# Kernel tuning notes

Measured on AMD Instinct MI355X. Metric: run time of the kernel, lower is better.

The kernel has to match this reference:

```python
import jax, jax.numpy as jnp
import numpy as np

N_HEADS = 8
EPS = 1e-5

def _mha(q_in, kv_in, wq, bq, wk, bk, wv, bv, wo, bo, causal):
    B, N, D = q_in.shape
    Dh = D // N_HEADS
    # projections (weights stored [in, out])
    Q = (q_in @ wq + bq).reshape(B, N, N_HEADS, Dh).swapaxes(1, 2)  # [B,H,N,Dh]
    K = (kv_in @ wk + bk).reshape(B, N, N_HEADS, Dh).swapaxes(1, 2)
    V = (kv_in @ wv + bv).reshape(B, N, N_HEADS, Dh).swapaxes(1, 2)
    scores = jnp.einsum('bhqd,bhkd->bhqk', Q, K) / jnp.sqrt(jnp.asarray(Dh, q_in.dtype))
    if causal:
        m = jnp.triu(jnp.ones((N, N), dtype=bool), k=1)
        scores = jnp.where(m, jnp.asarray(-jnp.inf, scores.dtype), scores)
    w = jax.nn.softmax(scores, axis=-1)
    attn = jnp.einsum('bhqk,bhkd->bhqd', w, V).swapaxes(1, 2).reshape(B, N, D)
    return attn @ wo + bo

def _ln(x, g, b):
    mu = jnp.mean(x, axis=-1, keepdims=True)
    var = jnp.var(x, axis=-1, keepdims=True)
    return (x - mu) / jnp.sqrt(var + EPS) * g + b

def setup_inputs() -> dict:
    key = jax.random.key(0)
    D, H, S = 512, 8, 4
    ks = jax.random.split(key, 32)
    def w(k, shape):
        return jax.random.normal(k, shape, dtype=jnp.float32) * 0.02
    inp = {
        'x': jax.random.normal(ks[0], (2, 2048, D), dtype=jnp.float32),
        'encoder_output': jax.random.normal(ks[1], (2, 2048, D), dtype=jnp.float32),
        # masked self-attention params
        'm_wq': w(ks[2], (D, D)), 'm_bq': jnp.zeros((D,), jnp.float32),
        'm_wk': w(ks[3], (D, D)), 'm_bk': jnp.zeros((D,), jnp.float32),
        'm_wv': w(ks[4], (D, D)), 'm_bv': jnp.zeros((D,), jnp.float32),
        'm_wo': w(ks[5], (D, D)), 'm_bo': jnp.zeros((D,), jnp.float32),
        # cross-attention params
        'c_wq': w(ks[6], (D, D)), 'c_bq': jnp.zeros((D,), jnp.float32),
        'c_wk': w(ks[7], (D, D)), 'c_bk': jnp.zeros((D,), jnp.float32),
        'c_wv': w(ks[8], (D, D)), 'c_bv': jnp.zeros((D,), jnp.float32),
        'c_wo': w(ks[9], (D, D)), 'c_bo': jnp.zeros((D,), jnp.float32),
        # layer norms
        'ln1_g': jnp.ones((D,), jnp.float32), 'ln1_b': jnp.zeros((D,), jnp.float32),
        'ln2_g': jnp.ones((D,), jnp.float32), 'ln2_b': jnp.zeros((D,), jnp.float32),
        'ln3_g': jnp.ones((D,), jnp.float32), 'ln3_b': jnp.zeros((D,), jnp.float32),
        # feed-forward (scale=4)
        'ff_w1': w(ks[10], (D, S * D)), 'ff_b1': jnp.zeros((S * D,), jnp.float32),
        'ff_w2': w(ks[11], (S * D, D)), 'ff_b2': jnp.zeros((D,), jnp.float32),
    }
    return inp

def reference(x, encoder_output,
              m_wq, m_bq, m_wk, m_bk, m_wv, m_bv, m_wo, m_bo,
              c_wq, c_bq, c_wk, c_bk, c_wv, c_bv, c_wo, c_bo,
              ln1_g, ln1_b, ln2_g, ln2_b, ln3_g, ln3_b,
              ff_w1, ff_b1, ff_w2, ff_b2):
    x = _mha(x, x, m_wq, m_bq, m_wk, m_bk, m_wv, m_bv, m_wo, m_bo, causal=True) + x
    x = _ln(x, ln1_g, ln1_b)
    x = _mha(x, encoder_output, c_wq, c_bq, c_wk, c_bk, c_wv, c_bv, c_wo, c_bo, causal=False) + x
    x = _ln(x, ln2_g, ln2_b)
    h = jax.nn.gelu(x @ ff_w1 + ff_b1, approximate=False)  # torch nn.GELU default = exact erf
    x = h @ ff_w2 + ff_b2 + x
    x = _ln(x, ln3_g, ln3_b)
    return x
```

## Files before the change

kernel.cpp:

```cpp
#include <hip/hip_runtime.h>
#include <hip/hip_bf16.h>

typedef __attribute__((ext_vector_type(8))) short short8;
typedef __attribute__((ext_vector_type(4))) float floatx4;
typedef unsigned short u16;
typedef unsigned int u32;

#define QSCALE 0.1803368801111244f

__device__ __forceinline__ u16 f2b(float f) {
    union { float f; u32 u; } v; v.f = f;
    u32 r = v.u + 0x7fffu + ((v.u >> 16) & 1u);
    return (u16)(r >> 16);
}

__device__ __forceinline__ float b2f(u16 b) {
    u32 u = ((u32)b) << 16;
    union { u32 u; float f; } v; v.u = u;
    return v.f;
}

__device__ __forceinline__ u32 pk2(float a, float b) {
    __hip_bfloat162 w = __float22bfloat162_rn(make_float2(a, b));
    return *(u32*)&w;
}

__device__ __forceinline__ void gload(const u16* g, u16* l) {
    __builtin_amdgcn_global_load_lds((const __attribute__((address_space(1))) void*)g,
                                     (__attribute__((address_space(3))) void*)l, 16, 0, 0);
}

struct TPent { const float* s; u16* d; int O; int dI; };
struct TP16 { TPent e[16]; };
__global__ __launch_bounds__(256) void transpose_convert16(TP16 p) {
    __shared__ float t[32][33];
    TPent e = p.e[blockIdx.z];
    int o0 = blockIdx.x * 32, i0 = blockIdx.y * 32;
    int tx = threadIdx.x, ty = threadIdx.y;
#pragma unroll
    for (int k = 0; k < 32; k += 8) t[ty + k][tx] = e.s[(size_t)(i0 + ty + k) * e.O + o0 + tx];
    __syncthreads();
#pragma unroll
    for (int k = 0; k < 32; k += 8) e.d[(size_t)(o0 + ty + k) * e.dI + i0 + tx] = f2b(t[tx][ty + k]);
}

__global__ __launch_bounds__(256) void gather_bias(const float* b0, const float* b1, const float* b2,
                                                   const float* b3, const float* b4,
                                                   float* dqkv, float* dkv) {
    int i = blockIdx.x * 256 + threadIdx.x;
    if      (i < 512)  dqkv[i] = b0[i];
    else if (i < 1024) dqkv[i] = b1[i - 512];
    else if (i < 1536) dqkv[i] = b2[i - 1024];
    else if (i < 2048) dkv[i - 1536] = b3[i - 1536];
    else               dkv[i - 1536] = b4[i - 2048];
}

__global__ __launch_bounds__(256) void cvt_bf16_2(const float4* __restrict__ s0, ushort4* __restrict__ d0,
                                                  const float4* __restrict__ s1, ushort4* __restrict__ d1) {
    int i = blockIdx.x * 256 + threadIdx.x;
    float4 v = s0[i];
    ushort4 o; o.x = f2b(v.x); o.y = f2b(v.y); o.z = f2b(v.z); o.w = f2b(v.w);
    d0[i] = o;
    v = s1[i];
    o.x = f2b(v.x); o.y = f2b(v.y); o.z = f2b(v.z); o.w = f2b(v.w);
    d1[i] = o;
}

__global__ __launch_bounds__(256) void gemm64x128(
    const u16* __restrict__ A, int lda,
    const u16* __restrict__ B, int ldb,
    int K,
    const float* __restrict__ bias,
    const float* __restrict__ residual,
    float* __restrict__ out_f, u16* __restrict__ out_b,
    int out_stride, int scale_ncols, int gelu_flag)
{
    __shared__ u16 lA[64 * 64];
    __shared__ u16 lB[128 * 64];
    int tid = threadIdx.x, wave = tid >> 6, lane = tid & 63;
    int g4 = lane >> 4, c16 = lane & 15;
    int swz = (c16 & 7) << 3;
    int bm = blockIdx.x * 64, bn = blockIdx.y * 128;
    int wm = (wave >> 1) * 32, wn = (wave & 1) * 64;
    int srow = tid >> 3, skseg = ((tid & 7) * 8) ^ ((srow & 7) << 3);
    const u16* Ar = A + (size_t)(bm + srow) * lda + skseg;
    const u16* Br = B + (size_t)(bn + srow) * ldb + skseg;
    size_t a32 = (size_t)32 * lda, b32 = (size_t)32 * ldb;

    floatx4 acc[2][4];
#pragma unroll
    for (int i = 0; i < 2; i++)
#pragma unroll
        for (int j = 0; j < 4; j++) acc[i][j] = (floatx4){0.f, 0.f, 0.f, 0.f};

    for (int kt = 0; kt < K; kt += 64) {
        __syncthreads();
        gload(Ar + kt,           lA + wave * 512);
        gload(Ar + kt + a32,     lA + 2048 + wave * 512);
        gload(Br + kt,           lB + wave * 512);
        gload(Br + kt + b32,     lB + 2048 + wave * 512);
        gload(Br + kt + 2 * b32, lB + 4096 + wave * 512);
        gload(Br + kt + 3 * b32, lB + 6144 + wave * 512);
        __syncthreads();
        short8 aF[2][2], bF[2][4];
#pragma unroll
        for (int kk = 0; kk < 2; kk++) {
            int ko = (g4 * 8 + kk * 32) ^ swz;
#pragma unroll
            for (int i = 0; i < 2; i++) aF[kk][i] = *(const short8*)&lA[(wm + i * 16 + c16) * 64 + ko];
#pragma unroll
            for (int j = 0; j < 4; j++) bF[kk][j] = *(const short8*)&lB[(wn + j * 16 + c16) * 64 + ko];
        }
#pragma unroll
        for (int kk = 0; kk < 2; kk++)
#pragma unroll
            for (int i = 0; i < 2; i++)
#pragma unroll
                for (int j = 0; j < 4; j++)
                    acc[i][j] = __builtin_amdgcn_mfma_f32_16x16x32_bf16(aF[kk][i], bF[kk][j], acc[i][j], 0, 0, 0);
    }

#pragma unroll
    for (int i = 0; i < 2; i++) {
        int row0 = bm + wm + i * 16 + g4 * 4;
#pragma unroll
        for (int j = 0; j < 4; j++) {
            int col = bn + wn + j * 16 + c16;
            float bv = bias[col];
#pragma unroll
            for (int r = 0; r < 4; r++) {
                int row = row0 + r;
                float v = acc[i][j][r] + bv;
                if (col < scale_ncols) v *= QSCALE;
                if (gelu_flag) v = 0.5f * v * (1.f + erff(v * 0.70710678118654752f));
                if (residual) v += residual[(size_t)row * out_stride + col];
                if (out_f) out_f[(size_t)row * out_stride + col] = v;
                else       out_b[(size_t)row * out_stride + col] = f2b(v);
            }
        }
    }
}

__global__ __launch_bounds__(256) void gemm64x128_dual(
    const u16* __restrict__ A0, const u16* __restrict__ B0, const float* __restrict__ bias0,
    u16* __restrict__ out0, int ostride0, int scale0,
    const u16* __restrict__ A1, const u16* __restrict__ B1, const float* __restrict__ bias1,
    u16* __restrict__ out1, int ostride1,
    int ys, int K, int lda, int ldb)
{
    __shared__ u16 lA[64 * 64];
    __shared__ u16 lB[128 * 64];
    int tid = threadIdx.x, wave = tid >> 6, lane = tid & 63;
    int g4 = lane >> 4, c16 = lane & 15;
    int swz = (c16 & 7) << 3;
    int by = blockIdx.y;
    const u16* A; const u16* B; const float* bias; u16* out; int ostride, scaleN, bn;
    if (by < ys) { A = A0; B = B0; bias = bias0; out = out0; ostride = ostride0; scaleN = scale0; bn = by * 128; }
    else         { A = A1; B = B1; bias = bias1; out = out1; ostride = ostride1; scaleN = 0;      bn = (by - ys) * 128; }
    int bm = blockIdx.x * 64;
    int wm = (wave >> 1) * 32, wn = (wave & 1) * 64;
    int srow = tid >> 3, skseg = ((tid & 7) * 8) ^ ((srow & 7) << 3);
    const u16* Ar = A + (size_t)(bm + srow) * lda + skseg;
    const u16* Br = B + (size_t)(bn + srow) * ldb + skseg;
    size_t a32 = (size_t)32 * lda, b32 = (size_t)32 * ldb;

    floatx4 acc[2][4];
#pragma unroll
    for (int i = 0; i < 2; i++)
#pragma unroll
        for (int j = 0; j < 4; j++) acc[i][j] = (floatx4){0.f, 0.f, 0.f, 0.f};

    for (int kt = 0; kt < K; kt += 64) {
        __syncthreads();
        gload(Ar + kt,           lA + wave * 512);
        gload(Ar + kt + a32,     lA + 2048 + wave * 512);
        gload(Br + kt,           lB + wave * 512);
        gload(Br + kt + b32,     lB + 2048 + wave * 512);
        gload(Br + kt + 2 * b32, lB + 4096 + wave * 512);
        gload(Br + kt + 3 * b32, lB + 6144 + wave * 512);
        __syncthreads();
        short8 aF[2][2], bF[2][4];
#pragma unroll
        for (int kk = 0; kk < 2; kk++) {
            int ko = (g4 * 8 + kk * 32) ^ swz;
#pragma unroll
            for (int i = 0; i < 2; i++) aF[kk][i] = *(const short8*)&lA[(wm + i * 16 + c16) * 64 + ko];
#pragma unroll
            for (int j = 0; j < 4; j++) bF[kk][j] = *(const short8*)&lB[(wn + j * 16 + c16) * 64 + ko];
        }
#pragma unroll
        for (int kk = 0; kk < 2; kk++)
#pragma unroll
            for (int i = 0; i < 2; i++)
#pragma unroll
                for (int j = 0; j < 4; j++)
                    acc[i][j] = __builtin_amdgcn_mfma_f32_16x16x32_bf16(aF[kk][i], bF[kk][j], acc[i][j], 0, 0, 0);
    }

#pragma unroll
    for (int i = 0; i < 2; i++) {
        int row0 = bm + wm + i * 16 + g4 * 4;
#pragma unroll
        for (int j = 0; j < 4; j++) {
            int col = bn + wn + j * 16 + c16;
            float bv = bias[col];
#pragma unroll
            for (int r = 0; r < 4; r++) {
                float v = acc[i][j][r] + bv;
                if (col < scaleN) v *= QSCALE;
                out[(size_t)(row0 + r) * ostride + col] = f2b(v);
            }
        }
    }
}

__global__ __launch_bounds__(256) void gemm64x64(
    const u16* __restrict__ A, int lda,
    const u16* __restrict__ B, int ldb,
    int K,
    const float* __restrict__ bias,
    u16* __restrict__ out_b,
    int out_stride, int scale_ncols)
{
    __shared__ u16 lA[64 * 64];
    __shared__ u16 lB[64 * 64];
    int tid = threadIdx.x, wave = tid >> 6, lane = tid & 63;
    int g4 = lane >> 4, c16 = lane & 15;
    int swz = (c16 & 7) << 3;
    int bm = blockIdx.x * 64, bn = blockIdx.y * 64;
    int wm = wave * 16;
    int srow = tid >> 3, skseg = ((tid & 7) * 8) ^ ((srow & 7) << 3);
    const u16* Ar = A + (size_t)(bm + srow) * lda + skseg;
    const u16* Br = B + (size_t)(bn + srow) * ldb + skseg;
    size_t a32 = (size_t)32 * lda, b32 = (size_t)32 * ldb;

    floatx4 acc[4];
#pragma unroll
    for (int j = 0; j < 4; j++) acc[j] = (floatx4){0.f, 0.f, 0.f, 0.f};

    for (int kt = 0; kt < K; kt += 64) {
        __syncthreads();
        gload(Ar + kt,       lA + wave * 512);
        gload(Ar + kt + a32, lA + 2048 + wave * 512);
        gload(Br + kt,       lB + wave * 512);
        gload(Br + kt + b32, lB + 2048 + wave * 512);
        __syncthreads();
        short8 aF[2], bF[2][4];
#pragma unroll
        for (int kk = 0; kk < 2; kk++) {
            int ko = (g4 * 8 + kk * 32) ^ swz;
            aF[kk] = *(const short8*)&lA[(wm + c16) * 64 + ko];
#pragma unroll
            for (int j = 0; j < 4; j++) bF[kk][j] = *(const short8*)&lB[(j * 16 + c16) * 64 + ko];
        }
#pragma unroll
        for (int kk = 0; kk < 2; kk++)
#pragma unroll
            for (int j = 0; j < 4; j++)
                acc[j] = __builtin_amdgcn_mfma_f32_16x16x32_bf16(aF[kk], bF[kk][j], acc[j], 0, 0, 0);
    }

    int row0 = bm + wm + g4 * 4;
#pragma unroll
    for (int j = 0; j < 4; j++) {
        int col = bn + j * 16 + c16;
        float bv = bias[col];
#pragma unroll
        for (int r = 0; r < 4; r++) {
            int row = row0 + r;
            float v = acc[j][r] + bv;
            if (col < scale_ncols) v *= QSCALE;
            out_b[(size_t)row * out_stride + col] = f2b(v);
        }
    }
}

__global__ __launch_bounds__(256) void gemm64x64s(
    const u16* __restrict__ A, int lda,
    const u16* __restrict__ B, int ldb,
    int Ksub,
    const float* __restrict__ bias,
    const float* __restrict__ res_f,
    const u16* __restrict__ res_b,
    u16* __restrict__ out0, int out_stride)
{
    __shared__ u16 lA[64 * 64];
    __shared__ u16 lB[64 * 64];
    int tid = threadIdx.x, wave = tid >> 6, lane = tid & 63;
    int g4 = lane >> 4, c16 = lane & 15;
    int swz = (c16 & 7) << 3;
    int bm = blockIdx.x * 64, bn = blockIdx.y * 64, sp = blockIdx.z;
    int wm = wave * 16;
    int srow = tid >> 3;
    int skseg = (((tid & 7) * 8) ^ ((srow & 7) << 3)) + sp * Ksub;
    const u16* Ar = A + (size_t)(bm + srow) * lda + skseg;
    const u16* Br = B + (size_t)(bn + srow) * ldb + skseg;
    size_t a32 = (size_t)32 * lda, b32 = (size_t)32 * ldb;

    floatx4 acc[4];
#pragma unroll
    for (int j = 0; j < 4; j++) acc[j] = (floatx4){0.f, 0.f, 0.f, 0.f};

    for (int kt = 0; kt < Ksub; kt += 64) {
        __syncthreads();
        gload(Ar + kt,       lA + wave * 512);
        gload(Ar + kt + a32, lA + 2048 + wave * 512);
        gload(Br + kt,       lB + wave * 512);
        gload(Br + kt + b32, lB + 2048 + wave * 512);
        __syncthreads();
        short8 aF[2], bF[2][4];
#pragma unroll
        for (int kk = 0; kk < 2; kk++) {
            int ko = (g4 * 8 + kk * 32) ^ swz;
            aF[kk] = *(const short8*)&lA[(wm + c16) * 64 + ko];
#pragma unroll
            for (int j = 0; j < 4; j++) bF[kk][j] = *(const short8*)&lB[(j * 16 + c16) * 64 + ko];
        }
#pragma unroll
        for (int kk = 0; kk < 2; kk++)
#pragma unroll
            for (int j = 0; j < 4; j++)
                acc[j] = __builtin_amdgcn_mfma_f32_16x16x32_bf16(aF[kk], bF[kk][j], acc[j], 0, 0, 0);
    }

    u16* out = out0 + (size_t)sp * 4096 * 512;
    int row0 = bm + wm + g4 * 4;
#pragma unroll
    for (int j = 0; j < 4; j++) {
        int col = bn + j * 16 + c16;
        float bv = (sp == 0) ? bias[col] : 0.f;
#pragma unroll
        for (int r = 0; r < 4; r++) {
            int row = row0 + r;
            float v = acc[j][r] + bv;
            if (sp == 0) {
                if (res_f)      v += res_f[(size_t)row * out_stride + col];
                else if (res_b) v += b2f(res_b[(size_t)row * out_stride + col]);
            }
            out[(size_t)row * out_stride + col] = f2b(v);
        }
    }
}

__global__ __launch_bounds__(256) void attn_fused(
    const u16* __restrict__ Qp, int q_stride,
    const u16* __restrict__ Kp, int kv_stride,
    const u16* __restrict__ Vp,
    u16* __restrict__ Opart,
    float* __restrict__ Lpart,
    int causal)
{
    __shared__ u16 lK[64 * 72];
    __shared__ u16 lVT[64 * 72];
    int tid = threadIdx.x, wave = tid >> 6, lane = tid & 63;
    int g4 = lane >> 4, c16 = lane & 15;
    int id = blockIdx.x;
    int bh = (id & 7) | ((id >> 3 & 1) << 3);
    int rest = id >> 4;
    int qt = rest & 31;
    int sp = rest >> 5;
    if (causal) qt = 31 - qt;
    size_t rowbase = (size_t)(bh >> 3) * 2048;
    int hoff = (bh & 7) * 64;
    const u16* Q = Qp + rowbase * q_stride + hoff;
    const u16* K = Kp + rowbase * kv_stride + hoff;
    const u16* V = Vp + rowbase * kv_stride + hoff;

    int qrow0 = qt * 64 + wave * 16;
    short8 qf0 = *(const short8*)&Q[(size_t)(qrow0 + c16) * q_stride + g4 * 8];
    short8 qf1 = *(const short8*)&Q[(size_t)(qrow0 + c16) * q_stride + g4 * 8 + 32];

    int kr = tid >> 2, ks = (tid & 3) * 16;
    int krow = 16 * (2 * (kr >> 5) + ((kr >> 2) & 1)) + 4 * ((kr >> 3) & 3) + (kr & 3);
    const u16* Kbase = K + (size_t)kr * kv_stride + ks;
    int vk0 = (tid >> 3) * 2, vs = (tid & 7) * 8;
    const u16* Vbase = V + (size_t)vk0 * kv_stride + vs;

    int4 kv0, kv1, vv0, vv1;
    auto load_tile = [&](int kt) {
        const u16* kp = Kbase + (size_t)kt * 64 * kv_stride;
        kv0 = *(const int4*)(kp);
        kv1 = *(const int4*)(kp + 8);
        const u16* vp = Vbase + (size_t)kt * 64 * kv_stride;
        vv0 = *(const int4*)(vp);
        vv1 = *(const int4*)(vp + kv_stride);
    };
    auto store_tile = [&]() {
        *(int4*)&lK[krow * 72 + ks] = kv0;
        *(int4*)&lK[krow * 72 + ks + 8] = kv1;
        const u16* pa = (const u16*)&vv0;
        const u16* pb = (const u16*)&vv1;
#pragma unroll
        for (int j = 0; j < 8; j++) {
            int dh = vs + j;
            int keyS = vk0 ^ (((dh >> 3) & 3) << 4);
            u32 w = (u32)pa[j] | ((u32)pb[j] << 16);
            *(u32*)&lVT[dh * 72 + keyS] = w;
        }
    };

    floatx4 o_acc[4];
#pragma unroll
    for (int d = 0; d < 4; d++) o_acc[d] = (floatx4){0.f, 0.f, 0.f, 0.f};
    float lsum = 0.f;

    int ktend = causal ? (qt + 1) : 32;
    int kt = sp;
    if (kt < ktend) load_tile(kt);

    for (; kt < ktend; kt += 2) {
        __syncthreads();
        store_tile();
        __syncthreads();
        if (kt + 2 < ktend) load_tile(kt + 2);

        floatx4 sc[4];
#pragma unroll
        for (int nt = 0; nt < 4; nt++) {
            short8 b0 = *(const short8*)&lK[(nt * 16 + c16) * 72 + g4 * 8];
            short8 b1 = *(const short8*)&lK[(nt * 16 + c16) * 72 + g4 * 8 + 32];
            floatx4 z = (floatx4){0.f, 0.f, 0.f, 0.f};
            z = __builtin_amdgcn_mfma_f32_16x16x32_bf16(b0, qf0, z, 0, 0, 0);
            z = __builtin_amdgcn_mfma_f32_16x16x32_bf16(b1, qf1, z, 0, 0, 0);
            sc[nt] = z;
        }
        if (causal && kt == qt) {
            int qr = qt * 64 + wave * 16 + c16;
#pragma unroll
            for (int nt = 0; nt < 4; nt++) {
                int key0 = kt * 64 + 8 * g4 + 4 * (nt & 1) + 32 * (nt >> 1);
#pragma unroll
                for (int r = 0; r < 4; r++)
                    if (key0 + r > qr) sc[nt][r] = -1e30f;
            }
        }
        float e[4][4];
#pragma unroll
        for (int nt = 0; nt < 4; nt++) {
#pragma unroll
            for (int r = 0; r < 4; r++) {
                e[nt][r] = exp2f(sc[nt][r]);
                lsum += e[nt][r];
            }
        }
        short8 pa0, pa1;
        {
            u32 w[8];
            w[0] = pk2(e[0][0], e[0][1]); w[1] = pk2(e[0][2], e[0][3]);
            w[2] = pk2(e[1][0], e[1][1]); w[3] = pk2(e[1][2], e[1][3]);
            w[4] = pk2(e[2][0], e[2][1]); w[5] = pk2(e[2][2], e[2][3]);
            w[6] = pk2(e[3][0], e[3][1]); w[7] = pk2(e[3][2], e[3][3]);
            pa0 = *(short8*)&w[0];
            pa1 = *(short8*)&w[4];
        }
#pragma unroll
        for (int d = 0; d < 4; d++) {
            int swz = ((2 * d + (c16 >> 3)) & 3) << 4;
            short8 vb0 = *(const short8*)&lVT[(d * 16 + c16) * 72 + ((g4 * 8) ^ swz)];
            short8 vb1 = *(const short8*)&lVT[(d * 16 + c16) * 72 + ((32 + g4 * 8) ^ swz)];
            o_acc[d] = __builtin_amdgcn_mfma_f32_16x16x32_bf16(pa0, vb0, o_acc[d], 0, 0, 0);
            o_acc[d] = __builtin_amdgcn_mfma_f32_16x16x32_bf16(pa1, vb1, o_acc[d], 0, 0, 0);
        }
    }

    lsum += __shfl_xor(lsum, 16);
    lsum += __shfl_xor(lsum, 32);
    size_t slab = (size_t)(sp * 16 + bh) * 2048;
    if (g4 == 0) Lpart[slab + qrow0 + c16] = lsum;
    u16* Ob = Opart + (slab + qrow0) * 64;
#pragma unroll
    for (int d = 0; d < 4; d++)
#pragma unroll
        for (int r = 0; r < 4; r++)
            Ob[(size_t)(4 * g4 + r) * 64 + d * 16 + c16] = f2b(o_acc[d][r]);
}

__global__ __launch_bounds__(256) void attn_combine(
    const ushort4* __restrict__ Op,
    const float* __restrict__ Lp,
    ushort4* __restrict__ out)
{
    int e = blockIdx.x * 256 + threadIdx.x;
    int dh4 = e & 15;
    int qrow = (e >> 4) & 2047;
    int bh = e >> 15;
    int li = bh * 2048 + qrow;
    float l = Lp[li] + Lp[32768 + li];
    float inv = 1.f / l;
    ushort4 a = Op[e];
    ushort4 b = Op[524288 + e];
    ushort4 o;
    o.x = f2b((b2f(a.x) + b2f(b.x)) * inv);
    o.y = f2b((b2f(a.y) + b2f(b.y)) * inv);
    o.z = f2b((b2f(a.z) + b2f(b.z)) * inv);
    o.w = f2b((b2f(a.w) + b2f(b.w)) * inv);
    int row = (bh >> 3) * 2048 + qrow;
    out[(size_t)row * 128 + (bh & 7) * 16 + dh4] = o;
}

__global__ __launch_bounds__(256) void ln_kernel(const u16* __restrict__ in0,
                                                 const u16* __restrict__ in1,
                                                 const float* __restrict__ g,
                                                 const float* __restrict__ b,
                                                 float* __restrict__ out_f,
                                                 u16* __restrict__ out_b)
{
    const int D = 512;
    int row = blockIdx.x, tid = threadIdx.x;
    size_t base = (size_t)row * D;
    float v0 = b2f(in0[base + tid]) + b2f(in1[base + tid]);
    float v1 = b2f(in0[base + tid + 256]) + b2f(in1[base + tid + 256]);
    float s = v0 + v1, ss = v0 * v0 + v1 * v1;
#pragma unroll
    for (int off = 1; off < 64; off <<= 1) { s += __shfl_xor(s, off); ss += __shfl_xor(ss, off); }
    __shared__ float red[8];
    int wave = tid >> 6, lane = tid & 63;
    if (lane == 0) { red[wave] = s; red[4 + wave] = ss; }
    __syncthreads();
    float st = red[0] + red[1] + red[2] + red[3];
    float sst = red[4] + red[5] + red[6] + red[7];
    float mu = st * (1.f / 512.f);
    float var = sst * (1.f / 512.f) - mu * mu;
    float rs = rsqrtf(var + 1e-5f);
    float y0 = (v0 - mu) * rs * g[tid] + b[tid];
    float y1 = (v1 - mu) * rs * g[tid + 256] + b[tid + 256];
    if (out_f) { out_f[base + tid] = y0; out_f[base + tid + 256] = y1; }
    if (out_b) { out_b[base + tid] = f2b(y0); out_b[base + tid + 256] = f2b(y1); }
}

extern "C" void kernel_launch(void* const* d_in, const int* in_sizes, int n_in,
                              void* d_out, int out_size, void* d_ws, size_t ws_size,
                              hipStream_t stream)
{
    (void)in_sizes; (void)n_in; (void)out_size; (void)ws_size;
    const float* x     = (const float*)d_in[0];
    const float* enc   = (const float*)d_in[1];
    const float* m_wq  = (const float*)d_in[2];  const float* m_bq = (const float*)d_in[3];
    const float* m_wk  = (const float*)d_in[4];  const float* m_bk = (const float*)d_in[5];
    const float* m_wv  = (const float*)d_in[6];  const float* m_bv = (const float*)d_in[7];
    const float* m_wo  = (const float*)d_in[8];  const float* m_bo = (const float*)d_in[9];
    const float* c_wq  = (const float*)d_in[10]; const float* c_bq = (const float*)d_in[11];
    const float* c_wk  = (const float*)d_in[12]; const float* c_bk = (const float*)d_in[13];
    const float* c_wv  = (const float*)d_in[14]; const float* c_bv = (const float*)d_in[15];
    const float* c_wo  = (const float*)d_in[16]; const float* c_bo = (const float*)d_in[17];
    const float* ln1_g = (const float*)d_in[18]; const float* ln1_b = (const float*)d_in[19];
    const float* ln2_g = (const float*)d_in[20]; const float* ln2_b = (const float*)d_in[21];
    const float* ln3_g = (const float*)d_in[22]; const float* ln3_b = (const float*)d_in[23];
    const float* ff_w1 = (const float*)d_in[24]; const float* ff_b1 = (const float*)d_in[25];
    const float* ff_w2 = (const float*)d_in[26]; const float* ff_b2 = (const float*)d_in[27];

    char* base = (char*)d_ws; size_t off = 0;
    auto alloc = [&](size_t bytes) -> void* {
        void* p = base + off; off = (off + bytes + 255) & ~(size_t)255; return p;
    };
    u16*   Wqkv_m = (u16*)alloc(1536 * 512 * 2);
    u16*   Wo_m   = (u16*)alloc(512 * 512 * 2);
    u16*   Wq_c   = (u16*)alloc(512 * 512 * 2);
    u16*   Wkv_c  = (u16*)alloc(1024 * 512 * 2);
    u16*   Wo_c   = (u16*)alloc(512 * 512 * 2);
    u16*   W1t    = (u16*)alloc(2048 * 512 * 2);
    u16*   W2t    = (u16*)alloc(512 * 2048 * 2);
    float* bqkv_m = (float*)alloc(1536 * 4);
    float* bkv_c  = (float*)alloc(1024 * 4);
    u16*   xb     = (u16*)alloc((size_t)4096 * 512 * 2);
    u16*   encb   = (u16*)alloc((size_t)4096 * 512 * 2);
    u16*   qkvm   = (u16*)alloc((size_t)4096 * 1536 * 2);
    u16*   attnm  = (u16*)alloc((size_t)4096 * 512 * 2);
    u16*   y01    = (u16*)alloc((size_t)2 * 4096 * 512 * 2);
    u16*   x1b    = (u16*)alloc((size_t)4096 * 512 * 2);
    u16*   qc     = (u16*)alloc((size_t)4096 * 512 * 2);
    u16*   kvc    = (u16*)alloc((size_t)4096 * 1024 * 2);
    u16*   attnc  = (u16*)alloc((size_t)4096 * 512 * 2);
    u16*   x2b    = (u16*)alloc((size_t)4096 * 512 * 2);
    u16*   h      = (u16*)alloc((size_t)4096 * 2048 * 2);
    u16*   Opart  = (u16*)alloc((size_t)2 * 16 * 2048 * 64 * 2);
    float* Lpart  = (float*)alloc((size_t)2 * 16 * 2048 * 4);

    TP16 tp;
    tp.e[0] = {m_wq, Wqkv_m,              512, 512};
    tp.e[1] = {m_wk, Wqkv_m + 512 * 512,  512, 512};
    tp.e[2] = {m_wv, Wqkv_m + 1024 * 512, 512, 512};
    tp.e[3] = {m_wo, Wo_m,                512, 512};
    tp.e[4] = {c_wq, Wq_c,                512, 512};
    tp.e[5] = {c_wk, Wkv_c,               512, 512};
    tp.e[6] = {c_wv, Wkv_c + 512 * 512,   512, 512};
    tp.e[7] = {c_wo, Wo_c,                512, 512};
    for (int k = 0; k < 4; k++)
        tp.e[8 + k]  = {ff_w1 + 512 * k,        W1t + k * 512 * 512, 2048, 512};
    for (int k = 0; k < 4; k++)
        tp.e[12 + k] = {ff_w2 + (size_t)512 * k * 512, W2t + 512 * k, 512, 2048};
    transpose_convert16<<<dim3(16, 16, 16), dim3(32, 8), 0, stream>>>(tp);
    gather_bias<<<10, 256, 0, stream>>>(m_bq, m_bk, m_bv, c_bk, c_bv, bqkv_m, bkv_c);
    cvt_bf16_2<<<2048, 256, 0, stream>>>((const float4*)x, (ushort4*)xb,
                                         (const float4*)enc, (ushort4*)encb);

    gemm64x128_dual<<<dim3(64, 20), 256, 0, stream>>>(
        xb, Wqkv_m, bqkv_m, qkvm, 1536, 512,
        encb, Wkv_c, bkv_c, kvc, 1024,
        12, 512, 512, 512);

    attn_fused<<<1024, 256, 0, stream>>>(qkvm, 1536, qkvm + 512, 1536, qkvm + 1024,
                                         Opart, Lpart, 1);
    attn_combine<<<2048, 256, 0, stream>>>((const ushort4*)Opart, Lpart, (ushort4*)attnm);
    gemm64x64s<<<dim3(64, 8, 2), 256, 0, stream>>>(attnm, 512, Wo_m, 512, 256,
                                                   m_bo, x, nullptr, y01, 512);
    ln_kernel<<<4096, 256, 0, stream>>>(y01, y01 + (size_t)4096 * 512, ln1_g, ln1_b,
                                        nullptr, x1b);

    gemm64x64<<<dim3(64, 8), 256, 0, stream>>>(x1b, 512, Wq_c, 512, 512,
                                               c_bq, qc, 512, 512);
    attn_fused<<<1024, 256, 0, stream>>>(qc, 512, kvc, 1024, kvc + 512,
                                         Opart, Lpart, 0);
    attn_combine<<<2048, 256, 0, stream>>>((const ushort4*)Opart, Lpart, (ushort4*)attnc);
    gemm64x64s<<<dim3(64, 8, 2), 256, 0, stream>>>(attnc, 512, Wo_c, 512, 256,
                                                   c_bo, nullptr, x1b, y01, 512);
    ln_kernel<<<4096, 256, 0, stream>>>(y01, y01 + (size_t)4096 * 512, ln2_g, ln2_b,
                                        nullptr, x2b);

    gemm64x128<<<dim3(64, 16), 256, 0, stream>>>(x2b, 512, W1t, 512, 512,
                                                 ff_b1, nullptr, nullptr, h, 2048, 0, 1);
    gemm64x64s<<<dim3(64, 8, 2), 256, 0, stream>>>(h, 2048, W2t, 2048, 1024,
                                                   ff_b2, nullptr, x2b, y01, 512);
    ln_kernel<<<4096, 256, 0, stream>>>(y01, y01 + (size_t)4096 * 512, ln3_g, ln3_b,
                                        (float*)d_out, nullptr);
}
```

Measured before the change: 299.7 us.

## Double-buffer GEMM K-tiles and split attention KV range four ways

```diff
diff --git a/kernel.cpp b/kernel.cpp
--- a/kernel.cpp
+++ b/kernel.cpp
@@ -75,17 +75,16 @@
     float* __restrict__ out_f, u16* __restrict__ out_b,
     int out_stride, int scale_ncols, int gelu_flag)
 {
-    __shared__ u16 lA[64 * 64];
-    __shared__ u16 lB[128 * 64];
+    __shared__ u16 lA[2 * 64 * 32];
+    __shared__ u16 lB[2 * 128 * 32];
     int tid = threadIdx.x, wave = tid >> 6, lane = tid & 63;
     int g4 = lane >> 4, c16 = lane & 15;
-    int swz = (c16 & 7) << 3;
     int bm = blockIdx.x * 64, bn = blockIdx.y * 128;
     int wm = (wave >> 1) * 32, wn = (wave & 1) * 64;
-    int srow = tid >> 3, skseg = ((tid & 7) * 8) ^ ((srow & 7) << 3);
+    int srow = tid >> 2, skseg = (tid & 3) * 8;
     const u16* Ar = A + (size_t)(bm + srow) * lda + skseg;
     const u16* Br = B + (size_t)(bn + srow) * ldb + skseg;
-    size_t a32 = (size_t)32 * lda, b32 = (size_t)32 * ldb;
+    size_t b64o = (size_t)64 * ldb;
 
     floatx4 acc[2][4];
 #pragma unroll
@@ -93,31 +92,31 @@
 #pragma unroll
         for (int j = 0; j < 4; j++) acc[i][j] = (floatx4){0.f, 0.f, 0.f, 0.f};
 
-    for (int kt = 0; kt < K; kt += 64) {
+    auto stage = [&](int buf, int kt) {
+        u16* dA = lA + buf * 2048 + wave * 512;
+        u16* dB = lB + buf * 4096 + wave * 512;
+        gload(Ar + kt, dA);
+        gload(Br + kt, dB);
+        gload(Br + kt + b64o, dB + 2048);
+    };
+
+    int cur = 0;
+    stage(0, 0);
+    __syncthreads();
+    for (int kt = 0; kt < K; kt += 32) {
+        if (kt + 32 < K) stage(cur ^ 1, kt + 32);
+        short8 aF[2], bF[4];
+#pragma unroll
+        for (int i = 0; i < 2; i++) aF[i] = *(const short8*)&lA[cur * 2048 + (wm + i * 16 + c16) * 32 + g4 * 8];
+#pragma unroll
+        for (int j = 0; j < 4; j++) bF[j] = *(const short8*)&lB[cur * 4096 + (wn + j * 16 + c16) * 32 + g4 * 8];
+#pragma unroll
+        for (int i = 0; i < 2; i++)
+#pragma unroll
+            for (int j = 0; j < 4; j++)
+                acc[i][j] = __builtin_amdgcn_mfma_f32_16x16x32_bf16(aF[i], bF[j], acc[i][j], 0, 0, 0);
         __syncthreads();
-        gload(Ar + kt,           lA + wave * 512);
-        gload(Ar + kt + a32,     lA + 2048 + wave * 512);
-        gload(Br + kt,           lB + wave * 512);
-        gload(Br + kt + b32,     lB + 2048 + wave * 512);
-        gload(Br + kt + 2 * b32, lB + 4096 + wave * 512);
-        gload(Br + kt + 3 * b32, lB + 6144 + wave * 512);
-        __syncthreads();
-        short8 aF[2][2], bF[2][4];
-#pragma unroll
-        for (int kk = 0; kk < 2; kk++) {
-            int ko = (g4 * 8 + kk * 32) ^ swz;
-#pragma unroll
-            for (int i = 0; i < 2; i++) aF[kk][i] = *(const short8*)&lA[(wm + i * 16 + c16) * 64 + ko];
-#pragma unroll
-            for (int j = 0; j < 4; j++) bF[kk][j] = *(const short8*)&lB[(wn + j * 16 + c16) * 64 + ko];
-        }
-#pragma unroll
-        for (int kk = 0; kk < 2; kk++)
-#pragma unroll
-            for (int i = 0; i < 2; i++)
-#pragma unroll
-                for (int j = 0; j < 4; j++)
-                    acc[i][j] = __builtin_amdgcn_mfma_f32_16x16x32_bf16(aF[kk][i], bF[kk][j], acc[i][j], 0, 0, 0);
+        cur ^= 1;
     }
 
 #pragma unroll
@@ -148,21 +147,20 @@
     u16* __restrict__ out1, int ostride1,
     int ys, int K, int lda, int ldb)
 {
-    __shared__ u16 lA[64 * 64];
-    __shared__ u16 lB[128 * 64];
+    __shared__ u16 lA[2 * 64 * 32];
+    __shared__ u16 lB[2 * 128 * 32];
     int tid = threadIdx.x, wave = tid >> 6, lane = tid & 63;
     int g4 = lane >> 4, c16 = lane & 15;
-    int swz = (c16 & 7) << 3;
     int by = blockIdx.y;
     const u16* A; const u16* B; const float* bias; u16* out; int ostride, scaleN, bn;
     if (by < ys) { A = A0; B = B0; bias = bias0; out = out0; ostride = ostride0; scaleN = scale0; bn = by * 128; }
     else         { A = A1; B = B1; bias = bias1; out = out1; ostride = ostride1; scaleN = 0;      bn = (by - ys) * 128; }
     int bm = blockIdx.x * 64;
     int wm = (wave >> 1) * 32, wn = (wave & 1) * 64;
-    int srow = tid >> 3, skseg = ((tid & 7) * 8) ^ ((srow & 7) << 3);
+    int srow = tid >> 2, skseg = (tid & 3) * 8;
     const u16* Ar = A + (size_t)(bm + srow) * lda + skseg;
     const u16* Br = B + (size_t)(bn + srow) * ldb + skseg;
-    size_t a32 = (size_t)32 * lda, b32 = (size_t)32 * ldb;
+    size_t b64o = (size_t)64 * ldb;
 
     floatx4 acc[2][4];
 #pragma unroll
@@ -170,31 +168,31 @@
 #pragma unroll
         for (int j = 0; j < 4; j++) acc[i][j] = (floatx4){0.f, 0.f, 0.f, 0.f};
 
-    for (int kt = 0; kt < K; kt += 64) {
+    auto stage = [&](int buf, int kt) {
+        u16* dA = lA + buf * 2048 + wave * 512;
+        u16* dB = lB + buf * 4096 + wave * 512;
+        gload(Ar + kt, dA);
+        gload(Br + kt, dB);
+        gload(Br + kt + b64o, dB + 2048);
+    };
+
+    int cur = 0;
+    stage(0, 0);
+    __syncthreads();
+    for (int kt = 0; kt < K; kt += 32) {
+        if (kt + 32 < K) stage(cur ^ 1, kt + 32);
+        short8 aF[2], bF[4];
+#pragma unroll
+        for (int i = 0; i < 2; i++) aF[i] = *(const short8*)&lA[cur * 2048 + (wm + i * 16 + c16) * 32 + g4 * 8];
+#pragma unroll
+        for (int j = 0; j < 4; j++) bF[j] = *(const short8*)&lB[cur * 4096 + (wn + j * 16 + c16) * 32 + g4 * 8];
+#pragma unroll
+        for (int i = 0; i < 2; i++)
+#pragma unroll
+            for (int j = 0; j < 4; j++)
+                acc[i][j] = __builtin_amdgcn_mfma_f32_16x16x32_bf16(aF[i], bF[j], acc[i][j], 0, 0, 0);
         __syncthreads();
-        gload(Ar + kt,           lA + wave * 512);
-        gload(Ar + kt + a32,     lA + 2048 + wave * 512);
-        gload(Br + kt,           lB + wave * 512);
-        gload(Br + kt + b32,     lB + 2048 + wave * 512);
-        gload(Br + kt + 2 * b32, lB + 4096 + wave * 512);
-        gload(Br + kt + 3 * b32, lB + 6144 + wave * 512);
-        __syncthreads();
-        short8 aF[2][2], bF[2][4];
-#pragma unroll
-        for (int kk = 0; kk < 2; kk++) {
-            int ko = (g4 * 8 + kk * 32) ^ swz;
-#pragma unroll
-            for (int i = 0; i < 2; i++) aF[kk][i] = *(const short8*)&lA[(wm + i * 16 + c16) * 64 + ko];
-#pragma unroll
-            for (int j = 0; j < 4; j++) bF[kk][j] = *(const short8*)&lB[(wn + j * 16 + c16) * 64 + ko];
-        }
-#pragma unroll
-        for (int kk = 0; kk < 2; kk++)
-#pragma unroll
-            for (int i = 0; i < 2; i++)
-#pragma unroll
-                for (int j = 0; j < 4; j++)
-                    acc[i][j] = __builtin_amdgcn_mfma_f32_16x16x32_bf16(aF[kk][i], bF[kk][j], acc[i][j], 0, 0, 0);
+        cur ^= 1;
     }
 
 #pragma unroll
@@ -222,42 +220,39 @@
     u16* __restrict__ out_b,
     int out_stride, int scale_ncols)
 {
-    __shared__ u16 lA[64 * 64];
-    __shared__ u16 lB[64 * 64];
+    __shared__ u16 lA[2 * 64 * 32];
+    __shared__ u16 lB[2 * 64 * 32];
     int tid = threadIdx.x, wave = tid >> 6, lane = tid & 63;
     int g4 = lane >> 4, c16 = lane & 15;
-    int swz = (c16 & 7) << 3;
     int bm = blockIdx.x * 64, bn = blockIdx.y * 64;
     int wm = wave * 16;
-    int srow = tid >> 3, skseg = ((tid & 7) * 8) ^ ((srow & 7) << 3);
+    int srow = tid >> 2, skseg = (tid & 3) * 8;
     const u16* Ar = A + (size_t)(bm + srow) * lda + skseg;
     const u16* Br = B + (size_t)(bn + srow) * ldb + skseg;
-    size_t a32 = (size_t)32 * lda, b32 = (size_t)32 * ldb;
 
     floatx4 acc[4];
 #pragma unroll
     for (int j = 0; j < 4; j++) acc[j] = (floatx4){0.f, 0.f, 0.f, 0.f};
 
-    for (int kt = 0; kt < K; kt += 64) {
+    auto stage = [&](int buf, int kt) {
+        gload(Ar + kt, lA + buf * 2048 + wave * 512);
+        gload(Br + kt, lB + buf * 2048 + wave * 512);
+    };
+
+    int cur = 0;
+    stage(0, 0);
+    __syncthreads();
+    for (int kt = 0; kt < K; kt += 32) {
+        if (kt + 32 < K) stage(cur ^ 1, kt + 32);
+        short8 aF = *(const short8*)&lA[cur * 2048 + (wm + c16) * 32 + g4 * 8];
+        short8 bF[4];
+#pragma unroll
+        for (int j = 0; j < 4; j++) bF[j] = *(const short8*)&lB[cur * 2048 + (j * 16 + c16) * 32 + g4 * 8];
+#pragma unroll
+        for (int j = 0; j < 4; j++)
+            acc[j] = __builtin_amdgcn_mfma_f32_16x16x32_bf16(aF, bF[j], acc[j], 0, 0, 0);
         __syncthreads();
-        gload(Ar + kt,       lA + wave * 512);
-        gload(Ar + kt + a32, lA + 2048 + wave * 512);
-        gload(Br + kt,       lB + wave * 512);
-        gload(Br + kt + b32, lB + 2048 + wave * 512);
-        __syncthreads();
-        short8 aF[2], bF[2][4];
-#pragma unroll
-        for (int kk = 0; kk < 2; kk++) {
-            int ko = (g4 * 8 + kk * 32) ^ swz;
-            aF[kk] = *(const short8*)&lA[(wm + c16) * 64 + ko];
-#pragma unroll
-            for (int j = 0; j < 4; j++) bF[kk][j] = *(const short8*)&lB[(j * 16 + c16) * 64 + ko];
-        }
-#pragma unroll
-        for (int kk = 0; kk < 2; kk++)
-#pragma unroll
-            for (int j = 0; j < 4; j++)
-                acc[j] = __builtin_amdgcn_mfma_f32_16x16x32_bf16(aF[kk], bF[kk][j], acc[j], 0, 0, 0);
+        cur ^= 1;
     }
 
     int row0 = bm + wm + g4 * 4;
@@ -284,43 +279,39 @@
     const u16* __restrict__ res_b,
     u16* __restrict__ out0, int out_stride)
 {
-    __shared__ u16 lA[64 * 64];
-    __shared__ u16 lB[64 * 64];
+    __shared__ u16 lA[2 * 64 * 32];
+    __shared__ u16 lB[2 * 64 * 32];
     int tid = threadIdx.x, wave = tid >> 6, lane = tid & 63;
     int g4 = lane >> 4, c16 = lane & 15;
-    int swz = (c16 & 7) << 3;
     int bm = blockIdx.x * 64, bn = blockIdx.y * 64, sp = blockIdx.z;
     int wm = wave * 16;
-    int srow = tid >> 3;
-    int skseg = (((tid & 7) * 8) ^ ((srow & 7) << 3)) + sp * Ksub;
+    int srow = tid >> 2, skseg = (tid & 3) * 8 + sp * Ksub;
     const u16* Ar = A + (size_t)(bm + srow) * lda + skseg;
     const u16* Br = B + (size_t)(bn + srow) * ldb + skseg;
-    size_t a32 = (size_t)32 * lda, b32 = (size_t)32 * ldb;
 
     floatx4 acc[4];
 #pragma unroll
     for (int j = 0; j < 4; j++) acc[j] = (floatx4){0.f, 0.f, 0.f, 0.f};
 
-    for (int kt = 0; kt < Ksub; kt += 64) {
+    auto stage = [&](int buf, int kt) {
+        gload(Ar + kt, lA + buf * 2048 + wave * 512);
+        gload(Br + kt, lB + buf * 2048 + wave * 512);
+    };
+
+    int cur = 0;
+    stage(0, 0);
+    __syncthreads();
+    for (int kt = 0; kt < Ksub; kt += 32) {
+        if (kt + 32 < Ksub) stage(cur ^ 1, kt + 32);
+        short8 aF = *(const short8*)&lA[cur * 2048 + (wm + c16) * 32 + g4 * 8];
+        short8 bF[4];
+#pragma unroll
+        for (int j = 0; j < 4; j++) bF[j] = *(const short8*)&lB[cur * 2048 + (j * 16 + c16) * 32 + g4 * 8];
+#pragma unroll
+        for (int j = 0; j < 4; j++)
+            acc[j] = __builtin_amdgcn_mfma_f32_16x16x32_bf16(aF, bF[j], acc[j], 0, 0, 0);
         __syncthreads();
-        gload(Ar + kt,       lA + wave * 512);
-        gload(Ar + kt + a32, lA + 2048 + wave * 512);
-        gload(Br + kt,       lB + wave * 512);
-        gload(Br + kt + b32, lB + 2048 + wave * 512);
-        __syncthreads();
-        short8 aF[2], bF[2][4];
-#pragma unroll
-        for (int kk = 0; kk < 2; kk++) {
-            int ko = (g4 * 8 + kk * 32) ^ swz;
-            aF[kk] = *(const short8*)&lA[(wm + c16) * 64 + ko];
-#pragma unroll
-            for (int j = 0; j < 4; j++) bF[kk][j] = *(const short8*)&lB[(j * 16 + c16) * 64 + ko];
-        }
-#pragma unroll
-        for (int kk = 0; kk < 2; kk++)
-#pragma unroll
-            for (int j = 0; j < 4; j++)
-                acc[j] = __builtin_amdgcn_mfma_f32_16x16x32_bf16(aF[kk], bF[kk][j], acc[j], 0, 0, 0);
+        cur ^= 1;
     }
 
     u16* out = out0 + (size_t)sp * 4096 * 512;
@@ -408,11 +399,11 @@
     int kt = sp;
     if (kt < ktend) load_tile(kt);
 
-    for (; kt < ktend; kt += 2) {
+    for (; kt < ktend; kt += 4) {
         __syncthreads();
         store_tile();
         __syncthreads();
-        if (kt + 2 < ktend) load_tile(kt + 2);
+        if (kt + 4 < ktend) load_tile(kt + 4);
 
         floatx4 sc[4];
 #pragma unroll
@@ -436,13 +427,14 @@
         }
         float e[4][4];
 #pragma unroll
-        for (int nt = 0; nt < 4; nt++) {
-#pragma unroll
-            for (int r = 0; r < 4; r++) {
-                e[nt][r] = exp2f(sc[nt][r]);
-                lsum += e[nt][r];
-            }
-        }
+        for (int nt = 0; nt < 4; nt++)
+#pragma unroll
+            for (int r = 0; r < 4; r++) e[nt][r] = exp2f(sc[nt][r]);
+        float s0 = (e[0][0] + e[0][1]) + (e[0][2] + e[0][3]);
+        float s1 = (e[1][0] + e[1][1]) + (e[1][2] + e[1][3]);
+        float s2 = (e[2][0] + e[2][1]) + (e[2][2] + e[2][3]);
+        float s3 = (e[3][0] + e[3][1]) + (e[3][2] + e[3][3]);
+        lsum += (s0 + s1) + (s2 + s3);
         short8 pa0, pa1;
         {
             u32 w[8];
@@ -485,15 +477,17 @@
     int qrow = (e >> 4) & 2047;
     int bh = e >> 15;
     int li = bh * 2048 + qrow;
-    float l = Lp[li] + Lp[32768 + li];
+    float l = (Lp[li] + Lp[32768 + li]) + (Lp[65536 + li] + Lp[98304 + li]);
     float inv = 1.f / l;
     ushort4 a = Op[e];
     ushort4 b = Op[524288 + e];
+    ushort4 c = Op[2 * 524288 + e];
+    ushort4 d = Op[3 * 524288 + e];
     ushort4 o;
-    o.x = f2b((b2f(a.x) + b2f(b.x)) * inv);
-    o.y = f2b((b2f(a.y) + b2f(b.y)) * inv);
-    o.z = f2b((b2f(a.z) + b2f(b.z)) * inv);
-    o.w = f2b((b2f(a.w) + b2f(b.w)) * inv);
+    o.x = f2b(((b2f(a.x) + b2f(b.x)) + (b2f(c.x) + b2f(d.x))) * inv);
+    o.y = f2b(((b2f(a.y) + b2f(b.y)) + (b2f(c.y) + b2f(d.y))) * inv);
+    o.z = f2b(((b2f(a.z) + b2f(b.z)) + (b2f(c.z) + b2f(d.z))) * inv);
+    o.w = f2b(((b2f(a.w) + b2f(b.w)) + (b2f(c.w) + b2f(d.w))) * inv);
     int row = (bh >> 3) * 2048 + qrow;
     out[(size_t)row * 128 + (bh & 7) * 16 + dh4] = o;
 }
@@ -573,8 +567,8 @@
     u16*   attnc  = (u16*)alloc((size_t)4096 * 512 * 2);
     u16*   x2b    = (u16*)alloc((size_t)4096 * 512 * 2);
     u16*   h      = (u16*)alloc((size_t)4096 * 2048 * 2);
-    u16*   Opart  = (u16*)alloc((size_t)2 * 16 * 2048 * 64 * 2);
-    float* Lpart  = (float*)alloc((size_t)2 * 16 * 2048 * 4);
+    u16*   Opart  = (u16*)alloc((size_t)4 * 16 * 2048 * 64 * 2);
+    float* Lpart  = (float*)alloc((size_t)4 * 16 * 2048 * 4);
 
     TP16 tp;
     tp.e[0] = {m_wq, Wqkv_m,              512, 512};
@@ -599,7 +593,7 @@
         encb, Wkv_c, bkv_c, kvc, 1024,
         12, 512, 512, 512);
 
-    attn_fused<<<1024, 256, 0, stream>>>(qkvm, 1536, qkvm + 512, 1536, qkvm + 1024,
+    attn_fused<<<2048, 256, 0, stream>>>(qkvm, 1536, qkvm + 512, 1536, qkvm + 1024,
                                          Opart, Lpart, 1);
     attn_combine<<<2048, 256, 0, stream>>>((const ushort4*)Opart, Lpart, (ushort4*)attnm);
     gemm64x64s<<<dim3(64, 8, 2), 256, 0, stream>>>(attnm, 512, Wo_m, 512, 256,
@@ -609,7 +603,7 @@
 
     gemm64x64<<<dim3(64, 8), 256, 0, stream>>>(x1b, 512, Wq_c, 512, 512,
                                                c_bq, qc, 512, 512);
-    attn_fused<<<1024, 256, 0, stream>>>(qc, 512, kvc, 1024, kvc + 512,
+    attn_fused<<<2048, 256, 0, stream>>>(qc, 512, kvc, 1024, kvc + 512,
                                          Opart, Lpart, 0);
     attn_combine<<<2048, 256, 0, stream>>>((const ushort4*)Opart, Lpart, (ushort4*)attnc);
     gemm64x64s<<<dim3(64, 8, 2), 256, 0, stream>>>(attnc, 512, Wo_c, 512, 256,
```

Result: slower. 315.8 us (+5.4%).
